# Performance work log

Measured on AMD Instinct MI355X. Metric: run time of the kernel, lower is better.

## Reference

```python
import jax, jax.numpy as jnp
import numpy as np

D = 256; HEADS = 8; HD = D // HEADS; LAYERS = 2
GS = 64; K = GS * GS; T = 4; P = 9; R = P // 2
B = 4; N = 511; H = 128; W = 128
SCALE = HD ** -0.5; SIGMA = 0.08


def _ln(x, g, b):
    m = jnp.mean(x, axis=-1, keepdims=True)
    v = jnp.var(x, axis=-1, keepdims=True)
    return (x - m) * jax.lax.rsqrt(v + 1e-5) * g + b


def _gelu(x):
    return jax.nn.gelu(x, approximate=False)  # torch nn.GELU default = exact erf


def _grid_xy():
    c = (jnp.arange(GS, dtype=jnp.float32) + 0.5) / GS
    gy, gx = jnp.meshgrid(c, c, indexing='ij')
    return jnp.stack([gx, gy], axis=-1).reshape(K, 2)  # (K,2)


def _patches(city, meas_xy):
    # city: (B,H,W), meas_xy: (B,N,2) -> (B,N,P,P)
    x = jnp.clip(jnp.round(meas_xy[..., 0] * (W - 1)).astype(jnp.int32), 0, W - 1)
    y = jnp.clip(jnp.round(meas_xy[..., 1] * (H - 1)).astype(jnp.int32), 0, H - 1)
    cp = jnp.pad(city, ((0, 0), (R, R), (R, R)))
    off = jnp.arange(P)  # = (-R..R) + R after padding
    yy = y[:, :, None, None] + off[None, None, :, None]
    xx = x[:, :, None, None] + off[None, None, None, :]
    bi = jnp.arange(B)[:, None, None, None]
    return cp[bi, yy, xx]


def _forward(meas_xy, meas_v, bs_xy, city, meas_W, meas_b, patch_W1, patch_b1,
             patch_W2, patch_b2, bs_W, bs_b, task_emb, taskp_W, taskp_b, grid_pos,
             lnq_g, lnq_b, lnkv_g, lnkv_b, qW, qb, kW, kb, vW, vb, oW, ob,
             dist_raw, dens_raw, lnf_g, lnf_b, f1W, f1b, f2W, f2b,
             tfp_W, tfp_b, head_W, head_b, task_id):
    # measurement tokens
    meas_in = jnp.concatenate([meas_xy, meas_v[..., None]], axis=-1)  # (B,N,3)
    meas_tok = meas_in @ meas_W + meas_b
    pf = _patches(city, meas_xy).reshape(B, N, P * P)
    pf = _gelu(pf @ patch_W1 + patch_b1) @ patch_W2 + patch_b2
    meas_tok = meas_tok + pf
    bs_tok = bs_xy @ bs_W + bs_b  # (B,1,D)
    src = jnp.concatenate([meas_tok, bs_tok], axis=1)          # (B,S,D)
    src_xy = jnp.concatenate([meas_xy, bs_xy], axis=1)         # (B,S,2)
    S = src.shape[1]

    gxy = _grid_xy()
    diff = gxy[None, :, None, :] - src_xy[:, None, :, :]       # (B,K,S,2)
    attn_bias = -jnp.sqrt(jnp.sum(diff * diff, axis=-1))       # (B,K,S)
    dm = gxy[None, :, None, :] - meas_xy[:, None, :, :]        # (B,K,N,2)
    density = jnp.mean(jnp.exp(-jnp.sum(dm * dm, axis=-1) / (2.0 * SIGMA * SIGMA)), axis=-1)  # (B,K)

    task_vec = (task_emb[task_id] @ taskp_W + taskp_b)[:, None, :]
    grid = grid_pos[None] + task_vec                           # (B,K,D)

    for i in range(LAYERS):
        q_in = _ln(grid, lnq_g[i], lnq_b[i])
        kv_in = _ln(src, lnkv_g[i], lnkv_b[i])
        q = (q_in @ qW[i] + qb[i]).reshape(B, K, HEADS, HD)
        k = (kv_in @ kW[i] + kb[i]).reshape(B, S, HEADS, HD)
        v = (kv_in @ vW[i] + vb[i]).reshape(B, S, HEADS, HD)
        scores = jnp.einsum('bkhd,bshd->bhks', q, k) * SCALE   # (B,H,K,S)
        scores = scores + jax.nn.softplus(dist_raw[i]) * attn_bias[:, None]
        gate = 1.0 + jnp.tanh(dens_raw[i]) * density[:, None, :, None]
        attn = jax.nn.softmax(scores * gate, axis=-1)
        out = jnp.einsum('bhks,bshd->bkhd', attn, v).reshape(B, K, D)
        grid = grid + out @ oW[i] + ob[i]
        hid = _ln(grid, lnf_g[i], lnf_b[i])
        grid = grid + _gelu(hid @ f1W[i] + f1b[i]) @ f2W[i] + f2b[i]

    tw = tfp_W[task_id]                                        # (B,D,D)
    tb = tfp_b[task_id]                                        # (B,D)
    tf = _gelu(jnp.einsum('bkd,bdh->bkh', grid, tw) + tb[:, None, :])
    logits = (tf @ head_W + head_b)[..., 0].reshape(B, GS, GS)
    return logits


def setup_inputs() -> dict:
    key = jax.random.key(0)
    ks = iter(jax.random.split(key, 48))
    def nrm(shape, s=0.02):
        return jax.random.normal(next(ks), shape, jnp.float32) * s
    inp = dict(
        meas_xy=jax.random.uniform(next(ks), (B, N, 2), jnp.float32),
        meas_v=jax.random.uniform(next(ks), (B, N), jnp.float32),
        bs_xy=jax.random.uniform(next(ks), (B, 1, 2), jnp.float32),
        city=jax.random.uniform(next(ks), (B, H, W), jnp.float32),
        meas_W=nrm((3, D)), meas_b=jnp.zeros(D),
        patch_W1=nrm((P * P, D)), patch_b1=jnp.zeros(D),
        patch_W2=nrm((D, D)), patch_b2=jnp.zeros(D),
        bs_W=nrm((2, D)), bs_b=jnp.zeros(D),
        task_emb=nrm((T, D), 1.0), taskp_W=nrm((D, D)), taskp_b=jnp.zeros(D),
        grid_pos=nrm((K, D)),
        lnq_g=jnp.ones((LAYERS, D)), lnq_b=jnp.zeros((LAYERS, D)),
        lnkv_g=jnp.ones((LAYERS, D)), lnkv_b=jnp.zeros((LAYERS, D)),
        qW=nrm((LAYERS, D, D)), qb=jnp.zeros((LAYERS, D)),
        kW=nrm((LAYERS, D, D)), kb=jnp.zeros((LAYERS, D)),
        vW=nrm((LAYERS, D, D)), vb=jnp.zeros((LAYERS, D)),
        oW=nrm((LAYERS, D, D)), ob=jnp.zeros((LAYERS, D)),
        dist_raw=nrm((LAYERS,), 0.5), dens_raw=nrm((LAYERS,), 0.5),
        lnf_g=jnp.ones((LAYERS, D)), lnf_b=jnp.zeros((LAYERS, D)),
        f1W=nrm((LAYERS, D, 2 * D)), f1b=jnp.zeros((LAYERS, 2 * D)),
        f2W=nrm((LAYERS, 2 * D, D)), f2b=jnp.zeros((LAYERS, D)),
        tfp_W=nrm((T, D, D)), tfp_b=jnp.zeros((T, D)),
        head_W=nrm((D, 1)), head_b=jnp.zeros(1),
        task_id=jax.random.randint(next(ks), (B,), 0, T),
    )
    return inp


def reference(meas_xy, meas_v, bs_xy, city, meas_W, meas_b, patch_W1, patch_b1,
              patch_W2, patch_b2, bs_W, bs_b, task_emb, taskp_W, taskp_b, grid_pos,
              lnq_g, lnq_b, lnkv_g, lnkv_b, qW, qb, kW, kb, vW, vb, oW, ob,
              dist_raw, dens_raw, lnf_g, lnf_b, f1W, f1b, f2W, f2b,
              tfp_W, tfp_b, head_W, head_b, task_id):
    return _forward(meas_xy, meas_v, bs_xy, city, meas_W, meas_b, patch_W1, patch_b1,
                    patch_W2, patch_b2, bs_W, bs_b, task_emb, taskp_W, taskp_b, grid_pos,
                    lnq_g, lnq_b, lnkv_g, lnkv_b, qW, qb, kW, kb, vW, vb, oW, ob,
                    dist_raw, dens_raw, lnf_g, lnf_b, f1W, f1b, f2W, f2b,
                    tfp_W, tfp_b, head_W, head_b, task_id)
```

## Files before the change

### kernel.cpp

```cpp
#include <hip/hip_runtime.h>
#include <hip/hip_fp16.h>
#include <math.h>

#define DD 256
#define NHEADS 8
#define HDIM 32
#define NLAYERS 2
#define GSZ 64
#define KGRID 4096
#define TTASK 4
#define BB 4
#define NMEAS 511
#define SSRC 512
#define HCITY 128
#define WCITY 128
#define ATT_SCALE 0.17677669529663687f
#define INV2S2 78.125f

typedef unsigned short u16;
typedef __attribute__((ext_vector_type(8))) short short8;
typedef __attribute__((ext_vector_type(4))) float f32x4;

__device__ __forceinline__ u16 f2bf(float f) {
    union { float f; unsigned int u; } x; x.f = f;
    return (u16)((x.u + 0x7fffu + ((x.u >> 16) & 1u)) >> 16);
}
__device__ __forceinline__ unsigned int cvtpk_bf16(float a, float b) {
    unsigned int r;
    asm("v_cvt_pk_bf16_f32 %0, %1, %2" : "=v"(r) : "v"(a), "v"(b));
    return r;
}
__device__ __forceinline__ float h2f(unsigned int u) {
    float r;
    asm("v_cvt_f32_f16 %0, %1" : "=v"(r) : "v"(u));
    return r;
}
__device__ __forceinline__ float gelu_f(float x) {
    return 0.5f * x * (1.0f + erff(x * 0.7071067811865476f));
}

__global__ void task_vec_kernel(const float* __restrict__ task_emb,
                                const float* __restrict__ tpW,
                                const float* __restrict__ tpb,
                                const int* __restrict__ task_id,
                                float* __restrict__ tv) {
    int b = blockIdx.x, t = threadIdx.x;
    int id = task_id[b];
    float a = tpb[t];
    for (int e = 0; e < DD; e++) a = fmaf(task_emb[id * DD + e], tpW[e * DD + t], a);
    tv[b * DD + t] = a;
}

__global__ void grid_init_kernel(const float* __restrict__ grid_pos,
                                 const float* __restrict__ tv,
                                 float* __restrict__ g) {
    int f = blockIdx.x * 256 + threadIdx.x;
    int b = f >> 18;
    float4 gp = ((const float4*)grid_pos)[f & 262143];
    float4 tvv = ((const float4*)tv)[b * 64 + (f & 63)];
    float4 o; o.x = gp.x + tvv.x; o.y = gp.y + tvv.y; o.z = gp.z + tvv.z; o.w = gp.w + tvv.w;
    ((float4*)g)[f] = o;
}

__global__ __launch_bounds__(256) void src_build_kernel(
    const float* __restrict__ meas_xy, const float* __restrict__ meas_v,
    const float* __restrict__ bs_xy, const float* __restrict__ city,
    const float* __restrict__ meas_W, const float* __restrict__ meas_b,
    const float* __restrict__ pW1, const float* __restrict__ pb1,
    const float* __restrict__ pW2, const float* __restrict__ pb2,
    const float* __restrict__ bs_W, const float* __restrict__ bs_b,
    float* __restrict__ src, float* __restrict__ src_xy) {
    __shared__ float sp[81];
    __shared__ float sh[DD];
    int b = blockIdx.x / SSRC, s = blockIdx.x % SSRC, t = threadIdx.x;
    if (s < NMEAS) {
        float mx = meas_xy[(b * NMEAS + s) * 2];
        float my = meas_xy[(b * NMEAS + s) * 2 + 1];
        float mv = meas_v[b * NMEAS + s];
        int cx = (int)rintf(mx * 127.0f); cx = min(max(cx, 0), 127);
        int cy = (int)rintf(my * 127.0f); cy = min(max(cy, 0), 127);
        if (t < 81) {
            int rr = cy + t / 9 - 4, cc = cx + t % 9 - 4;
            sp[t] = (rr >= 0 && rr < HCITY && cc >= 0 && cc < WCITY)
                        ? city[(b * HCITY + rr) * WCITY + cc] : 0.0f;
        }
        __syncthreads();
        float a1 = pb1[t];
        #pragma unroll 9
        for (int e = 0; e < 81; e++) a1 = fmaf(sp[e], pW1[e * DD + t], a1);
        sh[t] = gelu_f(a1);
        __syncthreads();
        float a2 = pb2[t];
        for (int e = 0; e < DD; e++) a2 = fmaf(sh[e], pW2[e * DD + t], a2);
        float mt = mx * meas_W[t] + my * meas_W[DD + t] + mv * meas_W[2 * DD + t] + meas_b[t];
        src[((size_t)(b * SSRC + s)) * DD + t] = mt + a2;
        if (t == 0) { src_xy[(b * SSRC + s) * 2] = mx; src_xy[(b * SSRC + s) * 2 + 1] = my; }
    } else {
        float bx = bs_xy[b * 2], by = bs_xy[b * 2 + 1];
        src[((size_t)(b * SSRC + s)) * DD + t] = bx * bs_W[t] + by * bs_W[DD + t] + bs_b[t];
        if (t == 0) { src_xy[(b * SSRC + s) * 2] = bx; src_xy[(b * SSRC + s) * 2 + 1] = by; }
    }
}

__global__ void density_kernel(const float* __restrict__ meas_xy, float* __restrict__ dens) {
    int w = threadIdx.x >> 6, lane = threadIdx.x & 63;
    int idx = blockIdx.x * 4 + w;
    int b = idx >> 12, k = idx & 4095;
    float gx = ((k & 63) + 0.5f) * (1.0f / 64.0f);
    float gy = ((k >> 6) + 0.5f) * (1.0f / 64.0f);
    float s = 0.0f;
    for (int n = lane; n < NMEAS; n += 64) {
        float2 xy = ((const float2*)meas_xy)[b * NMEAS + n];
        float dx = gx - xy.x, dy = gy - xy.y;
        s += __expf(-(dx * dx + dy * dy) * INV2S2);
    }
    #pragma unroll
    for (int o = 1; o < 64; o <<= 1) s += __shfl_xor(s, o, 64);
    if (lane == 0) dens[idx] = s * (1.0f / 511.0f);
}

__global__ __launch_bounds__(256) void dist_kernel(const float* __restrict__ sxy_g,
                                                   u16* __restrict__ dt) {
    __shared__ float2 sxy[SSRC];
    int bk = blockIdx.x;
    int b = bk >> 12, k = bk & 4095;
    int t = threadIdx.x;
    sxy[t]       = ((const float2*)sxy_g)[b * SSRC + t];
    sxy[t + 256] = ((const float2*)sxy_g)[b * SSRC + t + 256];
    __syncthreads();
    float gx = ((k & 63) + 0.5f) * (1.0f / 64.0f);
    float gy = ((k >> 6) + 0.5f) * (1.0f / 64.0f);
    float2 p0 = sxy[2 * t], p1 = sxy[2 * t + 1];
    float dx0 = gx - p0.x, dy0 = gy - p0.y;
    float dx1 = gx - p1.x, dy1 = gy - p1.y;
    float d0 = sqrtf(dx0 * dx0 + dy0 * dy0);
    float d1 = sqrtf(dx1 * dx1 + dy1 * dy1);
    __half h0 = __float2half(d0), h1 = __float2half(d1);
    unsigned int pk = (unsigned int)__half_as_ushort(h0) |
                      ((unsigned int)__half_as_ushort(h1) << 16);
    ((unsigned int*)dt)[(size_t)bk * 256 + t] = pk;
}

__global__ void ln_kernel(const float* __restrict__ X, const float* __restrict__ g,
                          const float* __restrict__ bvec, u16* __restrict__ Yb, int rows) {
    int w = threadIdx.x >> 6, lane = threadIdx.x & 63;
    int row = blockIdx.x * 4 + w;
    if (row >= rows) return;
    float4 x = ((const float4*)X)[(size_t)row * 64 + lane];
    float s = x.x + x.y + x.z + x.w;
    float q = x.x * x.x + x.y * x.y + x.z * x.z + x.w * x.w;
    #pragma unroll
    for (int o = 1; o < 64; o <<= 1) { s += __shfl_xor(s, o, 64); q += __shfl_xor(q, o, 64); }
    float m = s * (1.0f / 256.0f);
    float v = q * (1.0f / 256.0f) - m * m;
    float rs = rsqrtf(v + 1e-5f);
    float4 gg = ((const float4*)g)[lane], bb = ((const float4*)bvec)[lane];
    float4 y;
    y.x = (x.x - m) * rs * gg.x + bb.x;
    y.y = (x.y - m) * rs * gg.y + bb.y;
    y.z = (x.z - m) * rs * gg.z + bb.z;
    y.w = (x.w - m) * rs * gg.w + bb.w;
    uint2 o2;
    o2.x = cvtpk_bf16(y.x, y.y);
    o2.y = cvtpk_bf16(y.z, y.w);
    *(uint2*)&Yb[(size_t)row * 256 + lane * 4] = o2;
}

__global__ __launch_bounds__(256) void wconv_kernel(const float* __restrict__ W,
                                                    u16* __restrict__ Wt, int Kd, int Nd) {
    __shared__ float L[32][33];
    int z = blockIdx.z;
    size_t zoff = (size_t)z * Kd * Nd;
    int n0 = blockIdx.x * 32, k0 = blockIdx.y * 32;
    int tx = threadIdx.x, ty = threadIdx.y;
    #pragma unroll
    for (int yy = 0; yy < 4; yy++)
        L[tx][ty + 8 * yy] = W[zoff + (size_t)(k0 + ty + 8 * yy) * Nd + n0 + tx];
    __syncthreads();
    #pragma unroll
    for (int yy = 0; yy < 4; yy++)
        Wt[zoff + (size_t)(n0 + ty + 8 * yy) * Kd + k0 + tx] = f2bf(L[ty + 8 * yy][tx]);
}

__global__ __launch_bounds__(256) void vtrans_kernel(const u16* __restrict__ V,
                                                     u16* __restrict__ Vt) {
    __shared__ u16 L[32][33];
    int b = blockIdx.z;
    int n0 = blockIdx.x * 32, s0 = blockIdx.y * 32;
    int tx = threadIdx.x, ty = threadIdx.y;
    #pragma unroll
    for (int yy = 0; yy < 4; yy++)
        L[tx][ty + 8 * yy] = V[(size_t)(b * SSRC + s0 + ty + 8 * yy) * DD + n0 + tx];
    __syncthreads();
    #pragma unroll
    for (int yy = 0; yy < 4; yy++)
        Vt[(size_t)(b * DD + n0 + ty + 8 * yy) * SSRC + s0 + tx] = L[ty + 8 * yy][tx];
}

template <int ACT, int RES, int OBF, int OF32, int BATW, int KD>
__global__ __launch_bounds__(256) void gemm_lds(
    const u16* __restrict__ A, const u16* __restrict__ Wt,
    const float* __restrict__ bias, float* __restrict__ C, u16* __restrict__ Cb,
    int Nfull, const int* __restrict__ task_id, int wstride, int bstride) {
    __shared__ u16 sA[2][128][64];
    __shared__ u16 sB[2][64][64];
    int t = threadIdx.x;
    int w = t >> 6, lane = t & 63, lq = lane & 15, g = lane >> 4;
    int m0 = blockIdx.x * 128, n0 = blockIdx.y * 64;
    const u16* Wp = Wt;
    const float* bp = bias;
    if (BATW) {
        int id = task_id[m0 / KGRID];
        Wp += (size_t)id * wstride;
        bp += (size_t)id * bstride;
    }
    int ar = t >> 1, ah = (t & 1) * 4;
    int br = t >> 2, bq = (t & 3) * 2;
    const u16* Ag = A + (size_t)(m0 + ar) * KD + ah * 8;
    const u16* Bg = Wp + (size_t)(n0 + br) * KD + bq * 8;
    uint4 avr[4], bvr[2];
    #pragma unroll
    for (int i = 0; i < 4; i++) avr[i] = *(const uint4*)(Ag + i * 8);
    #pragma unroll
    for (int i = 0; i < 2; i++) bvr[i] = *(const uint4*)(Bg + i * 8);

    f32x4 acc[2][4];
    #pragma unroll
    for (int fm = 0; fm < 2; fm++)
        #pragma unroll
        for (int fn = 0; fn < 4; fn++) acc[fm][fn] = {0.f, 0.f, 0.f, 0.f};

    const int NK = KD / 64;
    #pragma unroll
    for (int ks = 0; ks < NK; ks++) {
        int cur = ks & 1;
        #pragma unroll
        for (int i = 0; i < 4; i++)
            *(uint4*)&sA[cur][ar][((ah + i) ^ (ar & 7)) * 8] = avr[i];
        #pragma unroll
        for (int i = 0; i < 2; i++)
            *(uint4*)&sB[cur][br][((bq + i) ^ (br & 7)) * 8] = bvr[i];
        if (ks + 1 < NK) {
            #pragma unroll
            for (int i = 0; i < 4; i++) avr[i] = *(const uint4*)(Ag + (ks + 1) * 64 + i * 8);
            #pragma unroll
            for (int i = 0; i < 2; i++) bvr[i] = *(const uint4*)(Bg + (ks + 1) * 64 + i * 8);
        }
        __syncthreads();
        #pragma unroll
        for (int sub = 0; sub < 2; sub++) {
            short8 af[2], bf[4];
            #pragma unroll
            for (int fm = 0; fm < 2; fm++)
                af[fm] = *(const short8*)&sA[cur][w * 32 + fm * 16 + lq][((sub * 4 + g) ^ (lq & 7)) * 8];
            #pragma unroll
            for (int fn = 0; fn < 4; fn++)
                bf[fn] = *(const short8*)&sB[cur][fn * 16 + lq][((sub * 4 + g) ^ (lq & 7)) * 8];
            #pragma unroll
            for (int fm = 0; fm < 2; fm++)
                #pragma unroll
                for (int fn = 0; fn < 4; fn++)
                    acc[fm][fn] = __builtin_amdgcn_mfma_f32_16x16x32_bf16(af[fm], bf[fn], acc[fm][fn], 0, 0, 0);
        }
        __syncthreads();
    }
    #pragma unroll
    for (int fm = 0; fm < 2; fm++) {
        int mbase = m0 + w * 32 + fm * 16 + 4 * g;
        #pragma unroll
        for (int fn = 0; fn < 4; fn++) {
            int col = n0 + fn * 16 + lq;
            float bv = bp[col];
            #pragma unroll
            for (int r = 0; r < 4; r++) {
                float o = acc[fm][fn][r] + bv;
                if (ACT) o = gelu_f(o);
                size_t off = (size_t)(mbase + r) * Nfull + col;
                if (RES) o += C[off];
                if (OF32) C[off] = o;
                if (OBF) Cb[off] = f2bf(o);
            }
        }
    }
}

#define DPAD 520
__global__ __launch_bounds__(512) void attn_mfma_kernel(
    const u16* __restrict__ Qb, const u16* __restrict__ Kb, const u16* __restrict__ Vt,
    const u16* __restrict__ distT, const float* __restrict__ dens,
    const float* __restrict__ dist_raw, const float* __restrict__ dens_raw,
    u16* __restrict__ O) {
    __shared__ u16 sD[32][DPAD];
    __shared__ u16 sP[16][512];
    int blk = blockIdx.x;
    int kt = blk & 127, b = blk >> 7;
    int t = threadIdx.x;
    {
        int r = t >> 4, cs = (t & 15) * 32;
        const u16* gp = distT + ((size_t)(b * KGRID) + kt * 32 + r) * SSRC + cs;
        uint4 d0 = *(const uint4*)gp;
        uint4 d1 = *(const uint4*)(gp + 8);
        uint4 d2 = *(const uint4*)(gp + 16);
        uint4 d3 = *(const uint4*)(gp + 24);
        *(uint4*)&sD[r][cs] = d0;
        *(uint4*)&sD[r][cs + 8] = d1;
        *(uint4*)&sD[r][cs + 16] = d2;
        *(uint4*)&sD[r][cs + 24] = d3;
    }
    __syncthreads();

    int w = t >> 6, lane = t & 63, lq = lane & 15, g = lane >> 4;
    int h = w;
    const float LOG2E = 1.4426950408889634f;
    float th = tanhf(dens_raw[0]);
    float c1 = log1pf(__expf(dist_raw[0]));
    float gs[2], gc[2];
    short8 qf[2];
    #pragma unroll
    for (int qc = 0; qc < 2; qc++) {
        int qrow = kt * 32 + qc * 16 + lq;
        float gate = 1.0f + th * dens[b * KGRID + qrow];
        gs[qc] = gate * ATT_SCALE * LOG2E;
        gc[qc] = gate * c1 * LOG2E;
        qf[qc] = *(const short8*)(Qb + (size_t)(b * KGRID + qrow) * DD + h * HDIM + g * 8);
    }
    const u16* kbase = Kb + (size_t)b * SSRC * DD + h * HDIM + g * 8;
    const u16* vbase = Vt + ((size_t)(b * NHEADS + h) * HDIM + lq) * SSRC + g * 8;

    f32x4 accA[2] = {{0.f, 0.f, 0.f, 0.f}, {0.f, 0.f, 0.f, 0.f}};
    f32x4 accB[2] = {{0.f, 0.f, 0.f, 0.f}, {0.f, 0.f, 0.f, 0.f}};
    f32x4 zero = {0.f, 0.f, 0.f, 0.f};
    float lsum[2] = {0.f, 0.f};

    for (int s0 = 0; s0 < SSRC; s0 += 32) {
        #pragma unroll
        for (int tl = 0; tl < 2; tl++) {
            int sb = s0 + tl * 16;
            short8 kf = *(const short8*)(kbase + (size_t)(sb + lq) * DD);
            #pragma unroll
            for (int qc = 0; qc < 2; qc++) {
                f32x4 c = __builtin_amdgcn_mfma_f32_16x16x32_bf16(kf, qf[qc], zero, 0, 0, 0);
                uint2 dh = *(const uint2*)&sD[qc * 16 + lq][sb + 4 * g];
                float p0 = exp2f(gs[qc] * c[0] - gc[qc] * h2f(dh.x));
                float p1 = exp2f(gs[qc] * c[1] - gc[qc] * h2f(dh.x >> 16));
                float p2 = exp2f(gs[qc] * c[2] - gc[qc] * h2f(dh.y));
                float p3 = exp2f(gs[qc] * c[3] - gc[qc] * h2f(dh.y >> 16));
                lsum[qc] += (p0 + p1) + (p2 + p3);
                int idx = lq * 32 + tl * 16 + 4 * g;
                *(unsigned int*)&sP[w * 2 + qc][idx]     = cvtpk_bf16(p0, p1);
                *(unsigned int*)&sP[w * 2 + qc][idx + 2] = cvtpk_bf16(p2, p3);
            }
        }
        short8 v0 = *(const short8*)(vbase + s0);
        short8 v1 = *(const short8*)(vbase + 16 * SSRC + s0);
        #pragma unroll
        for (int qc = 0; qc < 2; qc++) {
            short8 pf = *(const short8*)&sP[w * 2 + qc][lq * 32 + g * 8];
            accA[qc] = __builtin_amdgcn_mfma_f32_16x16x32_bf16(v0, pf, accA[qc], 0, 0, 0);
            accB[qc] = __builtin_amdgcn_mfma_f32_16x16x32_bf16(v1, pf, accB[qc], 0, 0, 0);
        }
    }

    #pragma unroll
    for (int qc = 0; qc < 2; qc++) {
        float ls = lsum[qc];
        ls += __shfl_xor(ls, 16, 64);
        ls += __shfl_xor(ls, 32, 64);
        float inv = 1.0f / ls;
        int qrow = kt * 32 + qc * 16 + lq;
        u16* op = O + (size_t)(b * KGRID + qrow) * DD + h * HDIM + 4 * g;
        uint2 o0, o1;
        o0.x = cvtpk_bf16(accA[qc][0] * inv, accA[qc][1] * inv);
        o0.y = cvtpk_bf16(accA[qc][2] * inv, accA[qc][3] * inv);
        o1.x = cvtpk_bf16(accB[qc][0] * inv, accB[qc][1] * inv);
        o1.y = cvtpk_bf16(accB[qc][2] * inv, accB[qc][3] * inv);
        *(uint2*)op = o0;
        *(uint2*)(op + 16) = o1;
    }
}

__global__ void head_kernel(const float* __restrict__ tf, const float* __restrict__ hW,
                            const float* __restrict__ hb, float* __restrict__ out) {
    int w = threadIdx.x >> 6, lane = threadIdx.x & 63;
    int idx = blockIdx.x * 4 + w;
    float4 x = ((const float4*)tf)[(size_t)idx * 64 + lane];
    float4 ww = ((const float4*)hW)[lane];
    float s = x.x * ww.x + x.y * ww.y + x.z * ww.z + x.w * ww.w;
    #pragma unroll
    for (int o = 1; o < 64; o <<= 1) s += __shfl_xor(s, o, 64);
    if (lane == 0) out[idx] = s + hb[0];
}

extern "C" void kernel_launch(void* const* d_in, const int* in_sizes, int n_in,
                              void* d_out, int out_size, void* d_ws, size_t ws_size,
                              hipStream_t stream) {
    const float* meas_xy = (const float*)d_in[0];
    const float* meas_v  = (const float*)d_in[1];
    const float* bs_xy   = (const float*)d_in[2];
    const float* city    = (const float*)d_in[3];
    const float* meas_W  = (const float*)d_in[4];
    const float* meas_b  = (const float*)d_in[5];
    const float* pW1     = (const float*)d_in[6];
    const float* pb1     = (const float*)d_in[7];
    const float* pW2     = (const float*)d_in[8];
    const float* pb2     = (const float*)d_in[9];
    const float* bs_W    = (const float*)d_in[10];
    const float* bs_b    = (const float*)d_in[11];
    const float* task_emb= (const float*)d_in[12];
    const float* taskp_W = (const float*)d_in[13];
    const float* taskp_b = (const float*)d_in[14];
    const float* grid_pos= (const float*)d_in[15];
    const float* lnq_g   = (const float*)d_in[16];
    const float* lnq_b   = (const float*)d_in[17];
    const float* lnkv_g  = (const float*)d_in[18];
    const float* lnkv_b  = (const float*)d_in[19];
    const float* qW      = (const float*)d_in[20];
    const float* qb      = (const float*)d_in[21];
    const float* kW      = (const float*)d_in[22];
    const float* kb      = (const float*)d_in[23];
    const float* vW      = (const float*)d_in[24];
    const float* vb      = (const float*)d_in[25];
    const float* oW      = (const float*)d_in[26];
    const float* ob      = (const float*)d_in[27];
    const float* dist_raw= (const float*)d_in[28];
    const float* dens_raw= (const float*)d_in[29];
    const float* lnf_g   = (const float*)d_in[30];
    const float* lnf_b   = (const float*)d_in[31];
    const float* f1W     = (const float*)d_in[32];
    const float* f1b     = (const float*)d_in[33];
    const float* f2W     = (const float*)d_in[34];
    const float* f2b     = (const float*)d_in[35];
    const float* tfp_W   = (const float*)d_in[36];
    const float* tfp_b   = (const float*)d_in[37];
    const float* head_W  = (const float*)d_in[38];
    const float* head_b  = (const float*)d_in[39];
    const int*   task_id = (const int*)d_in[40];

    float* ws = (float*)d_ws;
    float* src   = ws;
    float* gridb = src + 524288;
    float* tmp1  = gridb + 4194304;
    float* sxyb  = tmp1 + 4194304;
    float* densb = sxyb + 4096;
    float* tvec  = densb + 16384;

    u16* distT = (u16*)tmp1;

    u16* wtq  = (u16*)(tvec + 1024);
    u16* wtk  = wtq  + 131072;
    u16* wtv  = wtk  + 131072;
    u16* wto  = wtv  + 131072;
    u16* wtf1 = wto  + 131072;
    u16* wtf2 = wtf1 + 262144;
    u16* wtt  = wtf2 + 262144;
    u16* kvbf = wtt  + 262144;
    u16* lnbf = kvbf + 524288;
    u16* qbf  = lnbf + 4194304;
    u16* kbf  = qbf  + 4194304;
    u16* vbf  = kbf  + 524288;
    u16* vtbf = vbf  + 524288;
    u16* obf  = vtbf + 524288;
    u16* fhbf = obf  + 4194304;

    const dim3 B32x8(32, 8);

    task_vec_kernel<<<BB, 256, 0, stream>>>(task_emb, taskp_W, taskp_b, task_id, tvec);
    grid_init_kernel<<<4096, 256, 0, stream>>>(grid_pos, tvec, gridb);
    src_build_kernel<<<BB * SSRC, 256, 0, stream>>>(meas_xy, meas_v, bs_xy, city,
                                                    meas_W, meas_b, pW1, pb1, pW2, pb2,
                                                    bs_W, bs_b, src, sxyb);
    density_kernel<<<4096, 256, 0, stream>>>(meas_xy, densb);
    dist_kernel<<<BB * KGRID, 256, 0, stream>>>(sxyb, distT);

    wconv_kernel<<<dim3(8, 8, 2), B32x8, 0, stream>>>(qW, wtq, 256, 256);
    wconv_kernel<<<dim3(8, 8, 2), B32x8, 0, stream>>>(kW, wtk, 256, 256);
    wconv_kernel<<<dim3(8, 8, 2), B32x8, 0, stream>>>(vW, wtv, 256, 256);
    wconv_kernel<<<dim3(8, 8, 2), B32x8, 0, stream>>>(oW, wto, 256, 256);
    wconv_kernel<<<dim3(16, 8, 2), B32x8, 0, stream>>>(f1W, wtf1, 256, 512);
    wconv_kernel<<<dim3(8, 16, 2), B32x8, 0, stream>>>(f2W, wtf2, 512, 256);
    wconv_kernel<<<dim3(8, 8, 4), B32x8, 0, stream>>>(tfp_W, wtt, 256, 256);

    for (int i = 0; i < NLAYERS; i++) {
        const int w16 = i * 65536, bso = i * DD;
        ln_kernel<<<512, 256, 0, stream>>>(src, lnkv_g + bso, lnkv_b + bso, kvbf, 2048);
        gemm_lds<0, 0, 1, 0, 0, 256><<<dim3(16, 4), 256, 0, stream>>>(
            kvbf, wtk + w16, kb + bso, tmp1, kbf, 256, nullptr, 0, 0);
        gemm_lds<0, 0, 1, 0, 0, 256><<<dim3(16, 4), 256, 0, stream>>>(
            kvbf, wtv + w16, vb + bso, tmp1, vbf, 256, nullptr, 0, 0);
        vtrans_kernel<<<dim3(8, 16, 4), B32x8, 0, stream>>>(vbf, vtbf);
        ln_kernel<<<4096, 256, 0, stream>>>(gridb, lnq_g + bso, lnq_b + bso, lnbf, 16384);
        gemm_lds<0, 0, 1, 0, 0, 256><<<dim3(128, 4), 256, 0, stream>>>(
            lnbf, wtq + w16, qb + bso, tmp1, qbf, 256, nullptr, 0, 0);
        attn_mfma_kernel<<<BB * (KGRID / 32), 512, 0, stream>>>(
            qbf, kbf, vtbf, distT, densb, dist_raw + i, dens_raw + i, obf);
        gemm_lds<0, 1, 0, 1, 0, 256><<<dim3(128, 4), 256, 0, stream>>>(
            obf, wto + w16, ob + bso, gridb, obf, 256, nullptr, 0, 0);
        ln_kernel<<<4096, 256, 0, stream>>>(gridb, lnf_g + bso, lnf_b + bso, lnbf, 16384);
        gemm_lds<1, 0, 1, 0, 0, 256><<<dim3(128, 8), 256, 0, stream>>>(
            lnbf, wtf1 + i * 131072, f1b + i * 512, tmp1, fhbf, 512, nullptr, 0, 0);
        gemm_lds<0, 1, 1, 1, 0, 512><<<dim3(128, 4), 256, 0, stream>>>(
            fhbf, wtf2 + i * 131072, f2b + bso, gridb, lnbf, 256, nullptr, 0, 0);
    }

    gemm_lds<1, 0, 0, 1, 1, 256><<<dim3(128, 4), 256, 0, stream>>>(
        lnbf, wtt, tfp_b, tmp1, obf, 256, task_id, 65536, 256);
    head_kernel<<<4096, 256, 0, stream>>>(tmp1, head_W, head_b, (float*)d_out);
}
```

Before: 584.8 us.

## Rewrite GEMM with direct global-to-LDS loads and 128x128 tiles

```diff
diff --git a/kernel.cpp b/kernel.cpp
--- a/kernel.cpp
+++ b/kernel.cpp
@@ -37,6 +37,11 @@
 }
 __device__ __forceinline__ float gelu_f(float x) {
     return 0.5f * x * (1.0f + erff(x * 0.7071067811865476f));
+}
+__device__ __forceinline__ void gload16(const u16* g, u16* l) {
+    __builtin_amdgcn_global_load_lds(
+        (__attribute__((address_space(1))) void*)g,
+        (__attribute__((address_space(3))) void*)l, 16, 0, 0);
 }
 
 __global__ void task_vec_kernel(const float* __restrict__ task_emb,
@@ -198,15 +203,16 @@
 }
 
 template <int ACT, int RES, int OBF, int OF32, int BATW, int KD>
-__global__ __launch_bounds__(256) void gemm_lds(
+__global__ __launch_bounds__(256) void gemm_glds(
     const u16* __restrict__ A, const u16* __restrict__ Wt,
     const float* __restrict__ bias, float* __restrict__ C, u16* __restrict__ Cb,
     int Nfull, const int* __restrict__ task_id, int wstride, int bstride) {
-    __shared__ u16 sA[2][128][64];
-    __shared__ u16 sB[2][64][64];
+    __shared__ u16 sA[2][128][32];
+    __shared__ u16 sB[2][128][32];
     int t = threadIdx.x;
     int w = t >> 6, lane = t & 63, lq = lane & 15, g = lane >> 4;
-    int m0 = blockIdx.x * 128, n0 = blockIdx.y * 64;
+    int wr = w >> 1, wc = w & 1;
+    int m0 = blockIdx.x * 128, n0 = blockIdx.y * 128;
     const u16* Wp = Wt;
     const float* bp = bias;
     if (BATW) {
@@ -214,62 +220,57 @@
         Wp += (size_t)id * wstride;
         bp += (size_t)id * bstride;
     }
-    int ar = t >> 1, ah = (t & 1) * 4;
-    int br = t >> 2, bq = (t & 3) * 2;
-    const u16* Ag = A + (size_t)(m0 + ar) * KD + ah * 8;
-    const u16* Bg = Wp + (size_t)(n0 + br) * KD + bq * 8;
-    uint4 avr[4], bvr[2];
-    #pragma unroll
-    for (int i = 0; i < 4; i++) avr[i] = *(const uint4*)(Ag + i * 8);
-    #pragma unroll
-    for (int i = 0; i < 2; i++) bvr[i] = *(const uint4*)(Bg + i * 8);
-
-    f32x4 acc[2][4];
-    #pragma unroll
-    for (int fm = 0; fm < 2; fm++)
+    int srow = lane >> 2;
+    int scol = (lane & 3) * 8;
+    const u16* Ag0 = A  + (size_t)(m0 + w * 32 + srow) * KD + scol;
+    const u16* Ag1 = Ag0 + (size_t)16 * KD;
+    const u16* Bg0 = Wp + (size_t)(n0 + w * 32 + srow) * KD + scol;
+    const u16* Bg1 = Bg0 + (size_t)16 * KD;
+
+    f32x4 acc[4][4];
+    #pragma unroll
+    for (int fm = 0; fm < 4; fm++)
         #pragma unroll
         for (int fn = 0; fn < 4; fn++) acc[fm][fn] = {0.f, 0.f, 0.f, 0.f};
 
-    const int NK = KD / 64;
-    #pragma unroll
-    for (int ks = 0; ks < NK; ks++) {
+    const int NKS = KD / 32;
+    gload16(Ag0, &sA[0][w * 32][0]);
+    gload16(Ag1, &sA[0][w * 32 + 16][0]);
+    gload16(Bg0, &sB[0][w * 32][0]);
+    gload16(Bg1, &sB[0][w * 32 + 16][0]);
+    __syncthreads();
+
+    #pragma unroll
+    for (int ks = 0; ks < NKS; ks++) {
         int cur = ks & 1;
-        #pragma unroll
-        for (int i = 0; i < 4; i++)
-            *(uint4*)&sA[cur][ar][((ah + i) ^ (ar & 7)) * 8] = avr[i];
-        #pragma unroll
-        for (int i = 0; i < 2; i++)
-            *(uint4*)&sB[cur][br][((bq + i) ^ (br & 7)) * 8] = bvr[i];
-        if (ks + 1 < NK) {
-            #pragma unroll
-            for (int i = 0; i < 4; i++) avr[i] = *(const uint4*)(Ag + (ks + 1) * 64 + i * 8);
-            #pragma unroll
-            for (int i = 0; i < 2; i++) bvr[i] = *(const uint4*)(Bg + (ks + 1) * 64 + i * 8);
+        if (ks + 1 < NKS) {
+            int ko = (ks + 1) * 32;
+            gload16(Ag0 + ko, &sA[cur ^ 1][w * 32][0]);
+            gload16(Ag1 + ko, &sA[cur ^ 1][w * 32 + 16][0]);
+            gload16(Bg0 + ko, &sB[cur ^ 1][w * 32][0]);
+            gload16(Bg1 + ko, &sB[cur ^ 1][w * 32 + 16][0]);
         }
-        __syncthreads();
-        #pragma unroll
-        for (int sub = 0; sub < 2; sub++) {
-            short8 af[2], bf[4];
-            #pragma unroll
-            for (int fm = 0; fm < 2; fm++)
-                af[fm] = *(const short8*)&sA[cur][w * 32 + fm * 16 + lq][((sub * 4 + g) ^ (lq & 7)) * 8];
+        short8 af[4], bf[4];
+        #pragma unroll
+        for (int fm = 0; fm < 4; fm++)
+            af[fm] = *(const short8*)&sA[cur][wr * 64 + fm * 16 + lq][g * 8];
+        #pragma unroll
+        for (int fn = 0; fn < 4; fn++)
+            bf[fn] = *(const short8*)&sB[cur][wc * 64 + fn * 16 + lq][g * 8];
+        #pragma unroll
+        for (int fm = 0; fm < 4; fm++)
             #pragma unroll
             for (int fn = 0; fn < 4; fn++)
-                bf[fn] = *(const short8*)&sB[cur][fn * 16 + lq][((sub * 4 + g) ^ (lq & 7)) * 8];
-            #pragma unroll
-            for (int fm = 0; fm < 2; fm++)
-                #pragma unroll
-                for (int fn = 0; fn < 4; fn++)
-                    acc[fm][fn] = __builtin_amdgcn_mfma_f32_16x16x32_bf16(af[fm], bf[fn], acc[fm][fn], 0, 0, 0);
-        }
+                acc[fm][fn] = __builtin_amdgcn_mfma_f32_16x16x32_bf16(af[fm], bf[fn], acc[fm][fn], 0, 0, 0);
         __syncthreads();
     }
-    #pragma unroll
-    for (int fm = 0; fm < 2; fm++) {
-        int mbase = m0 + w * 32 + fm * 16 + 4 * g;
+
+    #pragma unroll
+    for (int fm = 0; fm < 4; fm++) {
+        int mbase = m0 + wr * 64 + fm * 16 + 4 * g;
         #pragma unroll
         for (int fn = 0; fn < 4; fn++) {
-            int col = n0 + fn * 16 + lq;
+            int col = n0 + wc * 64 + fn * 16 + lq;
             float bv = bp[col];
             #pragma unroll
             for (int r = 0; r < 4; r++) {
@@ -483,26 +484,26 @@
     for (int i = 0; i < NLAYERS; i++) {
         const int w16 = i * 65536, bso = i * DD;
         ln_kernel<<<512, 256, 0, stream>>>(src, lnkv_g + bso, lnkv_b + bso, kvbf, 2048);
-        gemm_lds<0, 0, 1, 0, 0, 256><<<dim3(16, 4), 256, 0, stream>>>(
+        gemm_glds<0, 0, 1, 0, 0, 256><<<dim3(16, 2), 256, 0, stream>>>(
             kvbf, wtk + w16, kb + bso, tmp1, kbf, 256, nullptr, 0, 0);
-        gemm_lds<0, 0, 1, 0, 0, 256><<<dim3(16, 4), 256, 0, stream>>>(
+        gemm_glds<0, 0, 1, 0, 0, 256><<<dim3(16, 2), 256, 0, stream>>>(
             kvbf, wtv + w16, vb + bso, tmp1, vbf, 256, nullptr, 0, 0);
         vtrans_kernel<<<dim3(8, 16, 4), B32x8, 0, stream>>>(vbf, vtbf);
         ln_kernel<<<4096, 256, 0, stream>>>(gridb, lnq_g + bso, lnq_b + bso, lnbf, 16384);
-        gemm_lds<0, 0, 1, 0, 0, 256><<<dim3(128, 4), 256, 0, stream>>>(
+        gemm_glds<0, 0, 1, 0, 0, 256><<<dim3(128, 2), 256, 0, stream>>>(
             lnbf, wtq + w16, qb + bso, tmp1, qbf, 256, nullptr, 0, 0);
         attn_mfma_kernel<<<BB * (KGRID / 32), 512, 0, stream>>>(
             qbf, kbf, vtbf, distT, densb, dist_raw + i, dens_raw + i, obf);
-        gemm_lds<0, 1, 0, 1, 0, 256><<<dim3(128, 4), 256, 0, stream>>>(
+        gemm_glds<0, 1, 0, 1, 0, 256><<<dim3(128, 2), 256, 0, stream>>>(
             obf, wto + w16, ob + bso, gridb, obf, 256, nullptr, 0, 0);
         ln_kernel<<<4096, 256, 0, stream>>>(gridb, lnf_g + bso, lnf_b + bso, lnbf, 16384);
-        gemm_lds<1, 0, 1, 0, 0, 256><<<dim3(128, 8), 256, 0, stream>>>(
+        gemm_glds<1, 0, 1, 0, 0, 256><<<dim3(128, 4), 256, 0, stream>>>(
             lnbf, wtf1 + i * 131072, f1b + i * 512, tmp1, fhbf, 512, nullptr, 0, 0);
-        gemm_lds<0, 1, 1, 1, 0, 512><<<dim3(128, 4), 256, 0, stream>>>(
+        gemm_glds<0, 1, 1, 1, 0, 512><<<dim3(128, 2), 256, 0, stream>>>(
             fhbf, wtf2 + i * 131072, f2b + bso, gridb, lnbf, 256, nullptr, 0, 0);
     }
 
-    gemm_lds<1, 0, 0, 1, 1, 256><<<dim3(128, 4), 256, 0, stream>>>(
+    gemm_glds<1, 0, 0, 1, 1, 256><<<dim3(128, 2), 256, 0, stream>>>(
         lnbf, wtt, tfp_b, tmp1, obf, 256, task_id, 65536, 256);
     head_kernel<<<4096, 256, 0, stream>>>(tmp1, head_W, head_b, (float*)d_out);
 }
```

After: 517.4 us. -11.5%, faster.
